# Kernel tuning notes

Measured on AMD Instinct MI355X. Metric: run time of the kernel, lower is better.

Reference implementation:

```python
import jax, jax.numpy as jnp
import numpy as np

B, N, D = 256, 128, 512
NUM_TYPES, NUM_STATS = 6, 8
W_TYPE, W_STATS, W_CORR = 1.0, 1.0, 0.5
LN_EPS = 1e-5


def setup_inputs() -> dict:
    key = jax.random.key(0)
    ks = jax.random.split(key, 20)
    s = 1.0 / np.sqrt(D)
    inp = {
        "column_embeddings": jax.random.normal(ks[0], (B, N, D), jnp.float32),
        "masked_columns": jax.random.bernoulli(ks[1], 0.15, (B, N)),
        "type_targets": jax.random.randint(ks[2], (N,), 0, NUM_TYPES),
        "column_statistics": jax.random.normal(ks[3], (B, N, NUM_STATS), jnp.float32),
        "column_correlations": jnp.tanh(jax.random.normal(ks[4], (B, N, N), jnp.float32)),
        # type head: Linear(D,D) -> GELU -> LayerNorm -> Linear(D,NUM_TYPES)
        "t_W1": jax.random.normal(ks[5], (D, D), jnp.float32) * s,
        "t_b1": jnp.zeros((D,), jnp.float32),
        "t_g": jnp.ones((D,), jnp.float32),
        "t_beta": jnp.zeros((D,), jnp.float32),
        "t_W2": jax.random.normal(ks[6], (D, NUM_TYPES), jnp.float32) * s,
        "t_b2": jnp.zeros((NUM_TYPES,), jnp.float32),
        # stats head
        "s_W1": jax.random.normal(ks[7], (D, D), jnp.float32) * s,
        "s_b1": jnp.zeros((D,), jnp.float32),
        "s_g": jnp.ones((D,), jnp.float32),
        "s_beta": jnp.zeros((D,), jnp.float32),
        "s_W2": jax.random.normal(ks[8], (D, NUM_STATS), jnp.float32) * s,
        "s_b2": jnp.zeros((NUM_STATS,), jnp.float32),
        # bilinear correlation: x_i^T W x_j + b
        "c_W": jax.random.normal(ks[9], (D, D), jnp.float32) * s,
        "c_b": jnp.zeros((), jnp.float32),
    }
    return inp


def _mlp_head(x, W1, b1, g, beta, W2, b2):
    h = jax.nn.gelu(x @ W1 + b1, approximate=False)
    mu = h.mean(-1, keepdims=True)
    var = ((h - mu) ** 2).mean(-1, keepdims=True)
    h = (h - mu) * jax.lax.rsqrt(var + LN_EPS) * g + beta
    return h @ W2 + b2


def _forward(column_embeddings, masked_columns, type_targets,
             column_statistics, column_correlations,
             t_W1, t_b1, t_g, t_beta, t_W2, t_b2,
             s_W1, s_b1, s_g, s_beta, s_W2, s_b2,
             c_W, c_b):
    e = column_embeddings  # [B,N,D]
    type_logits = _mlp_head(e, t_W1, t_b1, t_g, t_beta, t_W2, t_b2)   # [B,N,T]
    stats_preds = _mlp_head(e, s_W1, s_b1, s_g, s_beta, s_W2, s_b2)   # [B,N,S]

    # batched bilinear correlation: tanh(e_i W e_j + b), diag forced to 1
    u = jnp.einsum('bnd,de->bne', e, c_W)            # [B,N,D]
    corr = jnp.tanh(jnp.einsum('bne,bme->bnm', u, e) + c_b)  # [B,N,N]
    eye = jnp.eye(e.shape[1], dtype=corr.dtype)
    corr = corr * (1.0 - eye) + eye

    m = masked_columns.astype(jnp.float32)           # [B,N]
    n_masked = jnp.maximum(m.sum(), 1.0)

    # type loss: masked-mean cross entropy; targets broadcast over batch
    logp = jax.nn.log_softmax(type_logits, axis=-1)
    tgt = jnp.broadcast_to(type_targets[None, :], m.shape)
    ce = -jnp.take_along_axis(logp, tgt[..., None], axis=-1)[..., 0]  # [B,N]
    type_loss = (ce * m).sum() / n_masked

    # stats loss: masked-mean MSE over [B,N,S]
    se = (stats_preds - column_statistics) ** 2
    stats_loss = (se * m[..., None]).sum() / (n_masked * se.shape[-1])

    # correlation loss: mask_expanded = m_i | m_j
    me = jnp.maximum(m[:, :, None], m[:, None, :])   # [B,N,N]
    n_me = jnp.maximum(me.sum(), 1.0)
    ce2 = (corr - column_correlations) ** 2
    correlation_loss = (ce2 * me).sum() / n_me

    total = W_TYPE * type_loss + W_STATS * stats_loss + W_CORR * correlation_loss
    return total


def reference(column_embeddings, masked_columns, type_targets,
              column_statistics, column_correlations,
              t_W1, t_b1, t_g, t_beta, t_W2, t_b2,
              s_W1, s_b1, s_g, s_beta, s_W2, s_b2,
              c_W, c_b):
    return _forward(column_embeddings, masked_columns, type_targets,
                    column_statistics, column_correlations,
                    t_W1, t_b1, t_g, t_beta, t_W2, t_b2,
                    s_W1, s_b1, s_g, s_beta, s_W2, s_b2,
                    c_W, c_b)
```

## Files before the change

kernel.cpp:

```cpp
#include <hip/hip_runtime.h>
#include <math.h>

#define Bx 256
#define Nx 128
#define Dx 512
#define NTYPES 6
#define NSTATS 8
#define LN_EPS 1e-5f
#define CAP 8192

typedef __attribute__((ext_vector_type(8))) short frag8;
typedef __attribute__((ext_vector_type(4))) float f32x4;

__device__ __forceinline__ unsigned short f2bf(float f) {
    unsigned u = __float_as_uint(f);
    u += 0x7fff + ((u >> 16) & 1);
    return (unsigned short)(u >> 16);
}
__device__ __forceinline__ float bf2f(unsigned short s) {
    return __uint_as_float((unsigned)s << 16);
}

#define ASYNC16(g, l) __builtin_amdgcn_global_load_lds(                      \
    (const __attribute__((address_space(1))) void*)(g),                      \
    (__attribute__((address_space(3))) void*)(l), 16, 0, 0)

#define VWAIT(NIMM)                                                          \
    asm volatile("s_waitcnt vmcnt(" #NIMM ")" ::: "memory");                 \
    __builtin_amdgcn_sched_barrier(0);
#define BARX __builtin_amdgcn_s_barrier();

#define EB_OFF    0ULL
#define HC_OFF    33554432ULL
#define WT_OFF    67108864ULL
#define WTC_OFF   68157440ULL
#define WC_OFF    68681728ULL
#define LIST_OFF  69206016ULL
#define CNTS_OFF  69238784ULL
#define BASES_OFF 69239808ULL
#define CNTP_OFF  69240832ULL
#define ACC_OFF   69240848ULL
#define DONE_OFF  69240864ULL

__global__ __launch_bounds__(256) void k_prep(
    const float* __restrict__ e, const float* __restrict__ W0,
    const float* __restrict__ W1, const float* __restrict__ W2,
    unsigned short* __restrict__ Eb, unsigned short* __restrict__ Tcmb,
    unsigned short* __restrict__ Tc, unsigned short* __restrict__ Wc,
    const int* __restrict__ m, int* __restrict__ list,
    int* __restrict__ cnts, int* __restrict__ bases, int* cntp) {
    const int bid = blockIdx.x;
    const int t = threadIdx.x;
    if (bid < 256) {
        const int b = bid;
        const int r = b * Nx + t;
        int v = 0;
        if (t < 128) v = (m[r] != 0) ? 1 : 0;
        const unsigned long long bal = __ballot(v);
        const int wid = t >> 6, lane = t & 63;
        __shared__ int wcnt[2];
        __shared__ int base;
        if (lane == 0 && wid < 2) wcnt[wid] = __popcll(bal);
        __syncthreads();
        const int cnt = wcnt[0] + wcnt[1];
        if (t == 0) {
            base = atomicAdd(cntp, cnt);
            cnts[b] = cnt;
            bases[b] = base;
        }
        __syncthreads();
        if (t < 128 && v) {
            const int rank = __popcll(bal & ((1ULL << lane) - 1)) +
                             (wid ? wcnt[0] : 0);
            const int p = base + rank;
            if (p < CAP) list[p] = r;
        }
        return;
    }
    if (bid < 448) {
        const int lin = bid - 256;
        const int mid = lin >> 6;
        const int tl  = lin & 63;
        const int ti = tl >> 3, tj = tl & 7;
        const float* W = (mid == 0) ? W0 : (mid == 1) ? W1 : W2;
        unsigned short* T = (mid == 2) ? Tc : (Tcmb + mid * 262144);
        __shared__ float sh[64][65];
        const int c = t & 63;
        const int r4 = t >> 6;
#pragma unroll
        for (int rr = 0; rr < 16; ++rr) {
            const int row = rr * 4 + r4;
            sh[row][c] = W[(size_t)(ti * 64 + row) * Dx + tj * 64 + c];
        }
        __syncthreads();
#pragma unroll
        for (int rr = 0; rr < 16; ++rr) {
            const int col2 = rr * 4 + r4;
            T[(size_t)(tj * 64 + col2) * Dx + ti * 64 + c] = f2bf(sh[c][col2]);
        }
        return;
    }
    if (bid < 512) {
        const int base = (bid - 448) * 4096 + t * 16;
        const float4* src = (const float4*)(W2 + base);
        unsigned short o[16];
#pragma unroll
        for (int q = 0; q < 4; ++q) {
            const float4 v = src[q];
            o[q * 4 + 0] = f2bf(v.x); o[q * 4 + 1] = f2bf(v.y);
            o[q * 4 + 2] = f2bf(v.z); o[q * 4 + 3] = f2bf(v.w);
        }
        *(uint4*)(Wc + base) = *(const uint4*)(o);
        *(uint4*)(Wc + base + 8) = *(const uint4*)(o + 8);
        return;
    }
    const int r = (bid - 512) * 4 + (t >> 6);
    const int lane = t & 63;
    const float4* src = (const float4*)(e + (size_t)r * Dx);
    const float4 a = src[lane * 2];
    const float4 b = src[lane * 2 + 1];
    unsigned short u[8] = {f2bf(a.x), f2bf(a.y), f2bf(a.z), f2bf(a.w),
                           f2bf(b.x), f2bf(b.y), f2bf(b.z), f2bf(b.w)};
    ((uint4*)(Eb + (size_t)r * Dx))[lane] = *(const uint4*)u;
}

__global__ __launch_bounds__(512) void k_gemms(
    const unsigned short* __restrict__ Eb,
    const unsigned short* __restrict__ Wtcmb,
    const unsigned short* __restrict__ Wtc,
    const unsigned short* __restrict__ Wc,
    const float* __restrict__ bias0, const float* __restrict__ bias1,
    unsigned short* __restrict__ Hc,
    const int* __restrict__ list, const int* __restrict__ cntp) {
    __shared__ unsigned short As[2 * 4096];
    __shared__ unsigned short Bs[2 * 8192];
    const int bid = blockIdx.x;
    const int t = threadIdx.x;
    const int cnt = min(*cntp, CAP);
    const int rt = ((bid >> 6) << 3) | (bid & 7);
    const int row0 = rt << 7;
    if (row0 >= cnt) return;
    const int ct = (bid >> 3) & 7;
    const int col0 = ct << 8;
    const unsigned short* Bbase =
        (ct < 4) ? (Wtcmb + (size_t)ct * 256 * Dx)
      : (ct < 6) ? (Wtc + (size_t)(ct - 4) * 256 * Dx)
                 : (Wc + (size_t)(ct - 6) * 256 * Dx);
    const int kq = (t & 3) ^ ((t >> 3) & 3);
    const int ra = list[min(row0 + (t >> 2), cnt - 1)];
    const unsigned short* pA = Eb + (size_t)ra * Dx + kq * 8;
    const unsigned short* pB0 = Bbase + (size_t)(t >> 2) * Dx + kq * 8;
    const unsigned short* pB1 = pB0 + (size_t)128 * Dx;
    const int w = t >> 6, l = t & 63;
    const int wr = (w >> 2) * 64, wcol = (w & 3) * 64;
    const int quad = l >> 4, mr = l & 15;
    const int co = (quad ^ ((mr >> 1) & 3)) * 8;

#define MSTAGE(bf, k0)                                                       \
  { ASYNC16(pA + (k0), As + (bf) * 4096 + t * 8);                            \
    ASYNC16(pB0 + (k0), Bs + (bf) * 8192 + t * 8);                           \
    ASYNC16(pB1 + (k0), Bs + (bf) * 8192 + 4096 + t * 8); }

    f32x4 acc[4][4] = {};
    MSTAGE(0, 0);
    int buf = 0;
    for (int k = 0; k < 16; ++k) {
        if (k < 15) { MSTAGE(buf ^ 1, (k + 1) * 32); VWAIT(3); }
        else        { VWAIT(0); }
        BARX;
        frag8 af[4], bfv[4];
#pragma unroll
        for (int i = 0; i < 4; ++i)
            af[i] = *(const frag8*)&As[buf * 4096 + (wr + i * 16 + mr) * 32 + co];
#pragma unroll
        for (int j = 0; j < 4; ++j)
            bfv[j] = *(const frag8*)&Bs[buf * 8192 + (wcol + j * 16 + mr) * 32 + co];
        __builtin_amdgcn_s_setprio(1);
#pragma unroll
        for (int i = 0; i < 4; ++i)
#pragma unroll
            for (int j = 0; j < 4; ++j)
                acc[i][j] = __builtin_amdgcn_mfma_f32_16x16x32_bf16(
                    af[i], bfv[j], acc[i][j], 0, 0, 0);
        __builtin_amdgcn_s_setprio(0);
        if (k < 15) BARX;
        buf ^= 1;
    }
#pragma unroll
    for (int i = 0; i < 4; ++i)
#pragma unroll
        for (int j = 0; j < 4; ++j)
#pragma unroll
            for (int r = 0; r < 4; ++r) {
                const int row = row0 + wr + i * 16 + quad * 4 + r;
                const int col = col0 + wcol + j * 16 + mr;
                float v = acc[i][j][r];
                if (col < 1024) {
                    v += (col < 512) ? bias0[col] : bias1[col - 512];
                    v = 0.5f * v * (1.0f + erff(v * 0.70710678118654752f));
                }
                Hc[(size_t)row * 2048 + col] = f2bf(v);
            }
#undef MSTAGE
}

__global__ __launch_bounds__(256) void k_tail(
    const unsigned short* __restrict__ Eb,
    const float* __restrict__ Ct, const int* __restrict__ m,
    const float* __restrict__ cbp,
    const unsigned short* __restrict__ Hc,
    const float* __restrict__ tg, const float* __restrict__ tbeta,
    const float* __restrict__ tW2, const float* __restrict__ tb2,
    const float* __restrict__ sg, const float* __restrict__ sbeta,
    const float* __restrict__ sW2, const float* __restrict__ sb2,
    const int* __restrict__ list, const int* __restrict__ cnts,
    const int* __restrict__ bases, const int* __restrict__ cntp,
    const int* __restrict__ tgt, const float* __restrict__ stats,
    float* __restrict__ accs, int* __restrict__ done,
    float* __restrict__ out) {
    __shared__ unsigned short Elds[2 * 8192];
    __shared__ unsigned short Ulds[2 * 2048];
    __shared__ unsigned short Vlds[2 * 2048];
    __shared__ float mloc[128];
    __shared__ int lrow[128];
    __shared__ float redf[4][2];
    const int t = threadIdx.x;
    const int w = t >> 6, l = t & 63;
    const int quad = l >> 4, mr = l & 15;

    if (blockIdx.x < 256) {
        const int b = blockIdx.x;
        const int cnt = cnts[b];
        const int cbase = bases[b];
        if (t < 128) {
            mloc[t] = (m[b * Nx + t] != 0) ? 1.0f : 0.0f;
            lrow[t] = (t < cnt) ? (list[cbase + t] & (Nx - 1)) : 0;
        }
        __syncthreads();
        float T1 = 0.0f, T2 = 0.0f, Tov = 0.0f;
        const float cb = cbp[0];
        const float* Ctb = Ct + (size_t)b * Nx * Nx;
        if (cnt > 0) {
            const int kqE = (t & 7) ^ ((t >> 4) & 7);
            const size_t rb = (size_t)b * Nx;
            const unsigned short* pE0 = Eb + (rb + (t >> 3)) * Dx + kqE * 8;
            const unsigned short* pE1 = Eb + (rb + 32 + (t >> 3)) * Dx + kqE * 8;
            const unsigned short* pE2 = Eb + (rb + 64 + (t >> 3)) * Dx + kqE * 8;
            const unsigned short* pE3 = Eb + (rb + 96 + (t >> 3)) * Dx + kqE * 8;
            const int hw = t >> 7;
            const int t2 = t & 127;
            const int kq2 = (t2 & 7) ^ ((t2 >> 4) & 7);

            for (int c0 = 0; c0 < cnt; c0 += 32) {
                const int ntc = min(((cnt - c0) + 15) >> 4, 2);
                const int ur0 = min(c0 + (t2 >> 3), cnt - 1);
                const int ur1 = min(c0 + 16 + (t2 >> 3), cnt - 1);
                const unsigned short* pUV0 = Hc + (size_t)(cbase + ur0) * 2048
                                             + (hw ? 1536 : 1024) + kq2 * 8;
                const unsigned short* pUV1 = Hc + (size_t)(cbase + ur1) * 2048
                                             + (hw ? 1536 : 1024) + kq2 * 8;
                unsigned short* UVdst = hw ? Vlds : Ulds;

#define TSTAGE(bf, ph)                                                       \
  { ASYNC16(pE0 + (ph) * 64, Elds + (bf) * 8192 + t * 8);                    \
    ASYNC16(pE1 + (ph) * 64, Elds + (bf) * 8192 + 2048 + t * 8);             \
    ASYNC16(pE2 + (ph) * 64, Elds + (bf) * 8192 + 4096 + t * 8);             \
    ASYNC16(pE3 + (ph) * 64, Elds + (bf) * 8192 + 6144 + t * 8);             \
    ASYNC16(pUV0 + (ph) * 64, UVdst + (bf) * 2048 + t2 * 8);                 \
    ASYNC16(pUV1 + (ph) * 64, UVdst + (bf) * 2048 + 1024 + t2 * 8); }

                f32x4 ar[2][2] = {};
                f32x4 ac[2][2] = {};
                TSTAGE(0, 0);
                int buf = 0;
                for (int k = 0; k < 8; ++k) {
                    if (k < 7) { TSTAGE(buf ^ 1, k + 1); VWAIT(6); }
                    else       { VWAIT(0); }
                    BARX;
#pragma unroll
                    for (int ks = 0; ks < 2; ++ks) {
                        const int co = ((ks * 4 + quad) ^ ((mr >> 1) & 7)) * 8;
                        frag8 ef[2];
#pragma unroll
                        for (int eidx = 0; eidx < 2; ++eidx)
                            ef[eidx] = *(const frag8*)&Elds[buf * 8192 +
                                (w * 32 + eidx * 16 + mr) * 64 + co];
                        __builtin_amdgcn_s_setprio(1);
#pragma unroll
                        for (int it = 0; it < 2; ++it)
                            if (it < ntc) {
                                const frag8 uf = *(const frag8*)&Ulds[
                                    buf * 2048 + (it * 16 + mr) * 64 + co];
                                ar[it][0] = __builtin_amdgcn_mfma_f32_16x16x32_bf16(
                                    uf, ef[0], ar[it][0], 0, 0, 0);
                                ar[it][1] = __builtin_amdgcn_mfma_f32_16x16x32_bf16(
                                    uf, ef[1], ar[it][1], 0, 0, 0);
                            }
#pragma unroll
                        for (int jt = 0; jt < 2; ++jt)
                            if (jt < ntc) {
                                const frag8 vf = *(const frag8*)&Vlds[
                                    buf * 2048 + (jt * 16 + mr) * 64 + co];
                                ac[0][jt] = __builtin_amdgcn_mfma_f32_16x16x32_bf16(
                                    ef[0], vf, ac[0][jt], 0, 0, 0);
                                ac[1][jt] = __builtin_amdgcn_mfma_f32_16x16x32_bf16(
                                    ef[1], vf, ac[1][jt], 0, 0, 0);
                            }
                        __builtin_amdgcn_s_setprio(0);
                    }
                    if (k < 7) BARX;
                    buf ^= 1;
                }
#pragma unroll
                for (int it = 0; it < 2; ++it)
                    if (it < ntc) {
#pragma unroll
                        for (int eidx = 0; eidx < 2; ++eidx) {
                            const int j = w * 32 + eidx * 16 + mr;
#pragma unroll
                            for (int r = 0; r < 4; ++r) {
                                const int pos = c0 + it * 16 + quad * 4 + r;
                                if (pos < cnt) {
                                    const int i = lrow[pos];
                                    const float s = ar[it][eidx][r];
                                    const float c = (i == j) ? 1.0f
                                                             : tanhf(s + cb);
                                    const float d = c - Ctb[i * Nx + j];
                                    T1 += d * d;
                                    Tov += d * d * mloc[j];
                                }
                            }
                        }
                    }
#pragma unroll
                for (int jt = 0; jt < 2; ++jt)
                    if (jt < ntc) {
                        const int pos = c0 + jt * 16 + mr;
                        const int valid = (pos < cnt);
                        const int j = lrow[pos & 127];
#pragma unroll
                        for (int eidx = 0; eidx < 2; ++eidx) {
#pragma unroll
                            for (int r = 0; r < 4; ++r) {
                                if (valid) {
                                    const int i = w * 32 + eidx * 16 +
                                                  quad * 4 + r;
                                    const float s = ac[eidx][jt][r];
                                    const float c = (i == j) ? 1.0f
                                                             : tanhf(s + cb);
                                    const float d = c - Ctb[i * Nx + j];
                                    T2 += d * d;
                                }
                            }
                        }
                    }
#undef TSTAGE
            }
        }
        float lsum = T1 + T2 - Tov;
#pragma unroll
        for (int off = 32; off > 0; off >>= 1) lsum += __shfl_down(lsum, off);
        if (l == 0) redf[w][0] = lsum;
        __syncthreads();
        if (t == 0) {
            atomicAdd(&accs[2], redf[0][0] + redf[1][0] + redf[2][0] + redf[3][0]);
            const float c = (float)cnt;
            atomicAdd(&accs[3], 256.0f * c - c * c);
        }
    } else {
        const int blk = blockIdx.x - 256;
        const int cnt = min(*cntp, CAP);
        float ce_acc = 0.0f, sse_acc = 0.0f;
        for (int idx = blk * 4 + w; idx < cnt; idx += 256 * 4) {
            const int r = list[idx];
            const uint4 ut = ((const uint4*)(Hc + (size_t)idx * 2048))[l];
            const uint4 us = ((const uint4*)(Hc + (size_t)idx * 2048 + 512))[l];
            float a[8], b8[8];
            {
                const unsigned uu[4] = {ut.x, ut.y, ut.z, ut.w};
                const unsigned vv[4] = {us.x, us.y, us.z, us.w};
#pragma unroll
                for (int j = 0; j < 4; ++j) {
                    a[2 * j]      = bf2f((unsigned short)(uu[j] & 0xffff));
                    a[2 * j + 1]  = bf2f((unsigned short)(uu[j] >> 16));
                    b8[2 * j]     = bf2f((unsigned short)(vv[j] & 0xffff));
                    b8[2 * j + 1] = bf2f((unsigned short)(vv[j] >> 16));
                }
            }
            float st = 0, qt = 0, ss = 0, qs = 0;
#pragma unroll
            for (int j = 0; j < 8; ++j) {
                st += a[j]; qt += a[j] * a[j];
                ss += b8[j]; qs += b8[j] * b8[j];
            }
#pragma unroll
            for (int off = 32; off > 0; off >>= 1) {
                st += __shfl_xor(st, off); qt += __shfl_xor(qt, off);
                ss += __shfl_xor(ss, off); qs += __shfl_xor(qs, off);
            }
            const float mt = st * (1.0f / Dx);
            const float rt = rsqrtf(qt * (1.0f / Dx) - mt * mt + LN_EPS);
            const float ms = ss * (1.0f / Dx);
            const float rs = rsqrtf(qs * (1.0f / Dx) - ms * ms + LN_EPS);

            const int c0 = l * 8;
            float tp[6] = {}, sp[8] = {};
#pragma unroll
            for (int j = 0; j < 8; ++j) {
                const int c = c0 + j;
                const float nt2 = (a[j] - mt) * rt * tg[c] + tbeta[c];
#pragma unroll
                for (int k = 0; k < 6; ++k) tp[k] += nt2 * tW2[c * 6 + k];
                const float ns = (b8[j] - ms) * rs * sg[c] + sbeta[c];
#pragma unroll
                for (int k = 0; k < 8; ++k) sp[k] += ns * sW2[c * 8 + k];
            }
#pragma unroll
            for (int k = 0; k < 6; ++k)
#pragma unroll
                for (int off = 32; off > 0; off >>= 1) tp[k] += __shfl_down(tp[k], off);
#pragma unroll
            for (int k = 0; k < 8; ++k)
#pragma unroll
                for (int off = 32; off > 0; off >>= 1) sp[k] += __shfl_down(sp[k], off);

            if (l == 0) {
                float lg[6];
#pragma unroll
                for (int k = 0; k < 6; ++k) lg[k] = tp[k] + tb2[k];
                float mx = lg[0];
#pragma unroll
                for (int k = 1; k < 6; ++k) mx = fmaxf(mx, lg[k]);
                float se = 0.0f;
#pragma unroll
                for (int k = 0; k < 6; ++k) se += expf(lg[k] - mx);
                ce_acc += -(lg[tgt[r & (Nx - 1)]] - mx - logf(se));
                float sse = 0.0f;
#pragma unroll
                for (int k = 0; k < 8; ++k) {
                    const float d = sp[k] + sb2[k] - stats[(size_t)r * NSTATS + k];
                    sse += d * d;
                }
                sse_acc += sse;
            }
        }
        if (l == 0) { redf[w][0] = ce_acc; redf[w][1] = sse_acc; }
        __syncthreads();
        if (t == 0) {
            atomicAdd(&accs[0], redf[0][0] + redf[1][0] + redf[2][0] + redf[3][0]);
            atomicAdd(&accs[1], redf[0][1] + redf[1][1] + redf[2][1] + redf[3][1]);
        }
    }
    __syncthreads();
    if (t == 0) {
        __threadfence();
        const int old = atomicAdd(done, 1);
        if (old == 511) {
            __threadfence();
            const float CE  = atomicAdd(&accs[0], 0.0f);
            const float SSE = atomicAdd(&accs[1], 0.0f);
            const float CO  = atomicAdd(&accs[2], 0.0f);
            const float ME  = atomicAdd(&accs[3], 0.0f);
            const float nm = fmaxf((float)min(*cntp, CAP), 1.0f);
            out[0] = CE / nm + SSE / (nm * (float)NSTATS) +
                     0.5f * CO / fmaxf(ME, 1.0f);
        }
    }
}

extern "C" void kernel_launch(void* const* d_in, const int* in_sizes, int n_in,
                              void* d_out, int out_size, void* d_ws, size_t ws_size,
                              hipStream_t stream) {
    const float* e      = (const float*)d_in[0];
    const int*   mcols  = (const int*)d_in[1];
    const int*   ttgt   = (const int*)d_in[2];
    const float* stats  = (const float*)d_in[3];
    const float* corrT  = (const float*)d_in[4];
    const float* tW1    = (const float*)d_in[5];
    const float* tb1    = (const float*)d_in[6];
    const float* tg     = (const float*)d_in[7];
    const float* tbeta  = (const float*)d_in[8];
    const float* tW2    = (const float*)d_in[9];
    const float* tb2    = (const float*)d_in[10];
    const float* sW1    = (const float*)d_in[11];
    const float* sb1    = (const float*)d_in[12];
    const float* sg     = (const float*)d_in[13];
    const float* sbeta  = (const float*)d_in[14];
    const float* sW2    = (const float*)d_in[15];
    const float* sb2    = (const float*)d_in[16];
    const float* cW     = (const float*)d_in[17];
    const float* cb     = (const float*)d_in[18];
    float* out = (float*)d_out;

    char* ws = (char*)d_ws;
    unsigned short* Eb    = (unsigned short*)(ws + EB_OFF);
    unsigned short* Hc    = (unsigned short*)(ws + HC_OFF);
    unsigned short* Wtcmb = (unsigned short*)(ws + WT_OFF);
    unsigned short* Wtc   = (unsigned short*)(ws + WTC_OFF);
    unsigned short* Wc    = (unsigned short*)(ws + WC_OFF);
    int*   list  = (int*)(ws + LIST_OFF);
    int*   cnts  = (int*)(ws + CNTS_OFF);
    int*   bases = (int*)(ws + BASES_OFF);
    int*   cntp  = (int*)(ws + CNTP_OFF);
    float* accs  = (float*)(ws + ACC_OFF);
    int*   done  = (int*)(ws + DONE_OFF);

    hipMemsetAsync(ws + CNTP_OFF, 0, 48, stream);
    k_prep<<<8704, 256, 0, stream>>>(e, tW1, sW1, cW, Eb, Wtcmb, Wtc, Wc,
                                     mcols, list, cnts, bases, cntp);
    k_gemms<<<512, 512, 0, stream>>>(Eb, Wtcmb, Wtc, Wc, tb1, sb1, Hc,
                                     list, cntp);
    k_tail<<<512, 256, 0, stream>>>(Eb, corrT, mcols, cb, Hc,
                                    tg, tbeta, tW2, tb2, sg, sbeta, sW2, sb2,
                                    list, cnts, bases, cntp, ttgt, stats,
                                    accs, done, out);
}
```

Measured before the change: 225.9 us.

## Fuse GEMM and tail kernels into one launch with global flag dependencies

Merges the two kernels into one persistent-style launch. The GEMM blocks use smaller 128x128 tiles with 256 threads, and the tail blocks spin on global atomic counters until the GEMM column tiles they depend on have finished. This is meant to remove a kernel-launch boundary and let the correlation and head tail work overlap with the remaining GEMM tiles. It risks deadlock or stalls if spinning blocks get scheduled before the producer blocks. It also grows the shared-memory footprint of every block to the union size, which may reduce occupancy.

```diff
diff --git a/kernel.cpp b/kernel.cpp
--- a/kernel.cpp
+++ b/kernel.cpp
@@ -41,6 +41,8 @@
 #define CNTP_OFF  69240832ULL
 #define ACC_OFF   69240848ULL
 #define DONE_OFF  69240864ULL
+#define GFA_OFF   69240868ULL
+#define GFB_OFF   69240872ULL
 
 __global__ __launch_bounds__(256) void k_prep(
     const float* __restrict__ e, const float* __restrict__ W0,
@@ -124,91 +126,15 @@
     ((uint4*)(Eb + (size_t)r * Dx))[lane] = *(const uint4*)u;
 }
 
-__global__ __launch_bounds__(512) void k_gemms(
+__global__ __launch_bounds__(256) void k_main(
     const unsigned short* __restrict__ Eb,
     const unsigned short* __restrict__ Wtcmb,
     const unsigned short* __restrict__ Wtc,
     const unsigned short* __restrict__ Wc,
     const float* __restrict__ bias0, const float* __restrict__ bias1,
     unsigned short* __restrict__ Hc,
-    const int* __restrict__ list, const int* __restrict__ cntp) {
-    __shared__ unsigned short As[2 * 4096];
-    __shared__ unsigned short Bs[2 * 8192];
-    const int bid = blockIdx.x;
-    const int t = threadIdx.x;
-    const int cnt = min(*cntp, CAP);
-    const int rt = ((bid >> 6) << 3) | (bid & 7);
-    const int row0 = rt << 7;
-    if (row0 >= cnt) return;
-    const int ct = (bid >> 3) & 7;
-    const int col0 = ct << 8;
-    const unsigned short* Bbase =
-        (ct < 4) ? (Wtcmb + (size_t)ct * 256 * Dx)
-      : (ct < 6) ? (Wtc + (size_t)(ct - 4) * 256 * Dx)
-                 : (Wc + (size_t)(ct - 6) * 256 * Dx);
-    const int kq = (t & 3) ^ ((t >> 3) & 3);
-    const int ra = list[min(row0 + (t >> 2), cnt - 1)];
-    const unsigned short* pA = Eb + (size_t)ra * Dx + kq * 8;
-    const unsigned short* pB0 = Bbase + (size_t)(t >> 2) * Dx + kq * 8;
-    const unsigned short* pB1 = pB0 + (size_t)128 * Dx;
-    const int w = t >> 6, l = t & 63;
-    const int wr = (w >> 2) * 64, wcol = (w & 3) * 64;
-    const int quad = l >> 4, mr = l & 15;
-    const int co = (quad ^ ((mr >> 1) & 3)) * 8;
-
-#define MSTAGE(bf, k0)                                                       \
-  { ASYNC16(pA + (k0), As + (bf) * 4096 + t * 8);                            \
-    ASYNC16(pB0 + (k0), Bs + (bf) * 8192 + t * 8);                           \
-    ASYNC16(pB1 + (k0), Bs + (bf) * 8192 + 4096 + t * 8); }
-
-    f32x4 acc[4][4] = {};
-    MSTAGE(0, 0);
-    int buf = 0;
-    for (int k = 0; k < 16; ++k) {
-        if (k < 15) { MSTAGE(buf ^ 1, (k + 1) * 32); VWAIT(3); }
-        else        { VWAIT(0); }
-        BARX;
-        frag8 af[4], bfv[4];
-#pragma unroll
-        for (int i = 0; i < 4; ++i)
-            af[i] = *(const frag8*)&As[buf * 4096 + (wr + i * 16 + mr) * 32 + co];
-#pragma unroll
-        for (int j = 0; j < 4; ++j)
-            bfv[j] = *(const frag8*)&Bs[buf * 8192 + (wcol + j * 16 + mr) * 32 + co];
-        __builtin_amdgcn_s_setprio(1);
-#pragma unroll
-        for (int i = 0; i < 4; ++i)
-#pragma unroll
-            for (int j = 0; j < 4; ++j)
-                acc[i][j] = __builtin_amdgcn_mfma_f32_16x16x32_bf16(
-                    af[i], bfv[j], acc[i][j], 0, 0, 0);
-        __builtin_amdgcn_s_setprio(0);
-        if (k < 15) BARX;
-        buf ^= 1;
-    }
-#pragma unroll
-    for (int i = 0; i < 4; ++i)
-#pragma unroll
-        for (int j = 0; j < 4; ++j)
-#pragma unroll
-            for (int r = 0; r < 4; ++r) {
-                const int row = row0 + wr + i * 16 + quad * 4 + r;
-                const int col = col0 + wcol + j * 16 + mr;
-                float v = acc[i][j][r];
-                if (col < 1024) {
-                    v += (col < 512) ? bias0[col] : bias1[col - 512];
-                    v = 0.5f * v * (1.0f + erff(v * 0.70710678118654752f));
-                }
-                Hc[(size_t)row * 2048 + col] = f2bf(v);
-            }
-#undef MSTAGE
-}
-
-__global__ __launch_bounds__(256) void k_tail(
-    const unsigned short* __restrict__ Eb,
     const float* __restrict__ Ct, const int* __restrict__ m,
     const float* __restrict__ cbp,
-    const unsigned short* __restrict__ Hc,
     const float* __restrict__ tg, const float* __restrict__ tbeta,
     const float* __restrict__ tW2, const float* __restrict__ tb2,
     const float* __restrict__ sg, const float* __restrict__ sbeta,
@@ -217,19 +143,107 @@
     const int* __restrict__ bases, const int* __restrict__ cntp,
     const int* __restrict__ tgt, const float* __restrict__ stats,
     float* __restrict__ accs, int* __restrict__ done,
+    int* __restrict__ gfa, int* __restrict__ gfb,
     float* __restrict__ out) {
-    __shared__ unsigned short Elds[2 * 8192];
-    __shared__ unsigned short Ulds[2 * 2048];
-    __shared__ unsigned short Vlds[2 * 2048];
+    __shared__ unsigned short smem[24576];
     __shared__ float mloc[128];
     __shared__ int lrow[128];
     __shared__ float redf[4][2];
+    const int bid = blockIdx.x;
     const int t = threadIdx.x;
     const int w = t >> 6, l = t & 63;
     const int quad = l >> 4, mr = l & 15;
 
-    if (blockIdx.x < 256) {
-        const int b = blockIdx.x;
+    if (bid < 1024) {
+        const int cnt = min(*cntp, CAP);
+        const int rt = ((bid >> 7) << 3) | (bid & 7);
+        const int ct = (bid >> 3) & 15;
+        int* flag = (ct >= 8) ? gfb : gfa;
+        const int row0 = rt << 7;
+        if (row0 >= cnt) {
+            if (t == 0) atomicAdd(flag, 1);
+            return;
+        }
+        const int col0 = ct << 7;
+        const unsigned short* Bbase =
+            (ct < 8)  ? (Wtcmb + (size_t)ct * 128 * Dx)
+          : (ct < 12) ? (Wtc + (size_t)(ct - 8) * 128 * Dx)
+                      : (Wc + (size_t)(ct - 12) * 128 * Dx);
+        unsigned short* As = smem;
+        unsigned short* Bs = smem + 8192;
+        const int kq = (t & 3) ^ ((t >> 3) & 3);
+        const int ra0 = list[min(row0 + (t >> 2), cnt - 1)];
+        const int ra1 = list[min(row0 + 64 + (t >> 2), cnt - 1)];
+        const unsigned short* pA0 = Eb + (size_t)ra0 * Dx + kq * 8;
+        const unsigned short* pA1 = Eb + (size_t)ra1 * Dx + kq * 8;
+        const unsigned short* pB0 = Bbase + (size_t)(t >> 2) * Dx + kq * 8;
+        const unsigned short* pB1 = Bbase + (size_t)(64 + (t >> 2)) * Dx + kq * 8;
+        const int wr = (w >> 1) * 64, wcol = (w & 1) * 64;
+        const int co = (quad ^ ((mr >> 1) & 3)) * 8;
+
+#define GSTG(bf, k0)                                                         \
+  { ASYNC16(pA0 + (k0), As + (bf) * 4096 + t * 8);                           \
+    ASYNC16(pA1 + (k0), As + (bf) * 4096 + 2048 + t * 8);                    \
+    ASYNC16(pB0 + (k0), Bs + (bf) * 4096 + t * 8);                           \
+    ASYNC16(pB1 + (k0), Bs + (bf) * 4096 + 2048 + t * 8); }
+
+        f32x4 acc[4][4] = {};
+        GSTG(0, 0);
+        int buf = 0;
+        for (int k = 0; k < 16; ++k) {
+            if (k < 15) { GSTG(buf ^ 1, (k + 1) * 32); VWAIT(4); }
+            else        { VWAIT(0); }
+            BARX;
+            frag8 af[4], bfv[4];
+#pragma unroll
+            for (int i = 0; i < 4; ++i)
+                af[i] = *(const frag8*)&As[buf * 4096 + (wr + i * 16 + mr) * 32 + co];
+#pragma unroll
+            for (int j = 0; j < 4; ++j)
+                bfv[j] = *(const frag8*)&Bs[buf * 4096 + (wcol + j * 16 + mr) * 32 + co];
+            __builtin_amdgcn_s_setprio(1);
+#pragma unroll
+            for (int i = 0; i < 4; ++i)
+#pragma unroll
+                for (int j = 0; j < 4; ++j)
+                    acc[i][j] = __builtin_amdgcn_mfma_f32_16x16x32_bf16(
+                        af[i], bfv[j], acc[i][j], 0, 0, 0);
+            __builtin_amdgcn_s_setprio(0);
+            if (k < 15) BARX;
+            buf ^= 1;
+        }
+#pragma unroll
+        for (int i = 0; i < 4; ++i)
+#pragma unroll
+            for (int j = 0; j < 4; ++j)
+#pragma unroll
+                for (int r = 0; r < 4; ++r) {
+                    const int row = row0 + wr + i * 16 + quad * 4 + r;
+                    const int col = col0 + wcol + j * 16 + mr;
+                    float v = acc[i][j][r];
+                    if (ct < 8) {
+                        v += (col < 512) ? bias0[col] : bias1[col - 512];
+                        v = 0.5f * v * (1.0f + erff(v * 0.70710678118654752f));
+                    }
+                    Hc[(size_t)row * 2048 + col] = f2bf(v);
+                }
+#undef GSTG
+        __syncthreads();
+        if (t == 0) { __threadfence(); atomicAdd(flag, 1); }
+        return;
+    }
+
+    if (bid < 1280) {
+        if (t == 0) {
+            while (atomicAdd(gfb, 0) < 512) { }
+            __threadfence();
+        }
+        __syncthreads();
+        asm volatile("" ::: "memory");
+        unsigned short* Elds = smem;
+        unsigned short* Ulds = smem + 16384;
+        unsigned short* Vlds = smem + 20480;
+        const int b = bid - 1024;
         const int cnt = cnts[b];
         const int cbase = bases[b];
         if (t < 128) {
@@ -368,7 +382,13 @@
             atomicAdd(&accs[3], 256.0f * c - c * c);
         }
     } else {
-        const int blk = blockIdx.x - 256;
+        if (t == 0) {
+            while (atomicAdd(gfa, 0) < 512) { }
+            __threadfence();
+        }
+        __syncthreads();
+        asm volatile("" ::: "memory");
+        const int blk = bid - 1280;
         const int cnt = min(*cntp, CAP);
         float ce_acc = 0.0f, sse_acc = 0.0f;
         for (int idx = blk * 4 + w; idx < cnt; idx += 256 * 4) {
@@ -504,14 +524,15 @@
     int*   cntp  = (int*)(ws + CNTP_OFF);
     float* accs  = (float*)(ws + ACC_OFF);
     int*   done  = (int*)(ws + DONE_OFF);
+    int*   gfa   = (int*)(ws + GFA_OFF);
+    int*   gfb   = (int*)(ws + GFB_OFF);
 
     hipMemsetAsync(ws + CNTP_OFF, 0, 48, stream);
     k_prep<<<8704, 256, 0, stream>>>(e, tW1, sW1, cW, Eb, Wtcmb, Wtc, Wc,
                                      mcols, list, cnts, bases, cntp);
-    k_gemms<<<512, 512, 0, stream>>>(Eb, Wtcmb, Wtc, Wc, tb1, sb1, Hc,
-                                     list, cntp);
-    k_tail<<<512, 256, 0, stream>>>(Eb, corrT, mcols, cb, Hc,
-                                    tg, tbeta, tW2, tb2, sg, sbeta, sW2, sb2,
-                                    list, cnts, bases, cntp, ttgt, stats,
-                                    accs, done, out);
+    k_main<<<1536, 256, 0, stream>>>(Eb, Wtcmb, Wtc, Wc, tb1, sb1, Hc,
+                                     corrT, mcols, cb,
+                                     tg, tbeta, tW2, tb2, sg, sbeta, sW2, sb2,
+                                     list, cnts, bases, cntp, ttgt, stats,
+                                     accs, done, gfa, gfb, out);
 }
```

Result: slower. 284.4 us (+25.9%).
